# Kernel optimization log

Measured on AMD Instinct MI355X. Metric: run time of the kernel, lower is better.

The kernel has to match this reference:

```python
import jax, jax.numpy as jnp
import numpy as np
import math

C = 256
NUM_CLASSES = 80
NUM_CONVS = 4
GROUPS = 32
LEVEL_SHAPES = [(100, 152), (50, 76), (25, 38), (13, 19), (7, 10)]
BATCH = 2


def conv2d(x, w, b):
    # x: [N,C,H,W], w: [O,I,3,3] -> SAME padding, stride 1
    y = jax.lax.conv_general_dilated(x, w, window_strides=(1, 1), padding='SAME',
                                     dimension_numbers=('NCHW', 'OIHW', 'NCHW'))
    return y + b[None, :, None, None]


def group_norm(x, w, b, groups=GROUPS, eps=1e-5):
    N, Ch, H, W = x.shape
    xg = x.reshape(N, groups, Ch // groups, H, W)
    mu = jnp.mean(xg, axis=(2, 3, 4), keepdims=True)
    var = jnp.var(xg, axis=(2, 3, 4), keepdims=True)
    xg = (xg - mu) * jax.lax.rsqrt(var + eps)
    x = xg.reshape(N, Ch, H, W)
    return x * w[None, :, None, None] + b[None, :, None, None]


def tower(x, cw, cb, gw, gb):
    for i in range(NUM_CONVS):
        x = jax.nn.relu(group_norm(conv2d(x, cw[i], cb[i]), gw[i], gb[i]))
    return x


def flatten_head(y, c):
    # [N, A*c, H, W] -> [N, H*W*A, c]  (matches view/permute/reshape in torch)
    N, AC, H, W = y.shape
    A = AC // c
    return y.reshape(N, A, c, H, W).transpose(0, 3, 4, 1, 2).reshape(N, H * W * A, c)


def setup_inputs() -> dict:
    key = jax.random.key(0)
    ks = iter(jax.random.split(key, 64))
    inp = {}
    for i, (h, w) in enumerate(LEVEL_SHAPES):
        inp[f"feat{i}"] = jax.random.normal(next(ks), (BATCH, C, h, w), jnp.float32)
    def cw(shape):  # conv weights init std=0.01 as in torch module
        return jax.random.normal(next(ks), shape, jnp.float32) * 0.01
    inp["cls_conv_w"] = cw((NUM_CONVS, C, C, 3, 3))
    inp["cls_conv_b"] = jnp.zeros((NUM_CONVS, C), jnp.float32)
    inp["cls_gn_w"] = jnp.ones((NUM_CONVS, C), jnp.float32)
    inp["cls_gn_b"] = jnp.zeros((NUM_CONVS, C), jnp.float32)
    inp["cls_out_w"] = cw((NUM_CLASSES, C, 3, 3))
    inp["cls_out_b"] = jnp.full((NUM_CLASSES,), -math.log(99.0), jnp.float32)  # prior prob 0.01
    inp["reg_conv_w"] = cw((NUM_CONVS, C, C, 3, 3))
    inp["reg_conv_b"] = jnp.zeros((NUM_CONVS, C), jnp.float32)
    inp["reg_gn_w"] = jnp.ones((NUM_CONVS, C), jnp.float32)
    inp["reg_gn_b"] = jnp.zeros((NUM_CONVS, C), jnp.float32)
    for name, oc in [("bbox", 4), ("ctr", 1), ("dim", 3), ("ori", 1), ("kp", 16), ("depth", 1)]:
        inp[f"{name}_w"] = cw((oc, C, 3, 3))
        inp[f"{name}_b"] = jnp.zeros((oc,), jnp.float32)
    return inp


def reference(feat0, feat1, feat2, feat3, feat4,
              cls_conv_w, cls_conv_b, cls_gn_w, cls_gn_b, cls_out_w, cls_out_b,
              reg_conv_w, reg_conv_b, reg_gn_w, reg_gn_b,
              bbox_w, bbox_b, ctr_w, ctr_b, dim_w, dim_b,
              ori_w, ori_b, kp_w, kp_b, depth_w, depth_b):
    feats = [feat0, feat1, feat2, feat3, feat4]
    cls_all, bbox_all, ctr_all, dim_all, ori_all, kp_all, depth_all = ([] for _ in range(7))
    for f in feats:
        cf = tower(f, cls_conv_w, cls_conv_b, cls_gn_w, cls_gn_b)
        cls_all.append(flatten_head(conv2d(cf, cls_out_w, cls_out_b), NUM_CLASSES))
        rf = tower(f, reg_conv_w, reg_conv_b, reg_gn_w, reg_gn_b)
        bbox_all.append(flatten_head(jax.nn.relu(conv2d(rf, bbox_w, bbox_b)), 4))
        ctr_all.append(flatten_head(conv2d(rf, ctr_w, ctr_b), 1))
        dim_all.append(flatten_head(conv2d(rf, dim_w, dim_b), 3))
        ori_all.append(flatten_head(conv2d(rf, ori_w, ori_b), 1))
        kp_all.append(flatten_head(conv2d(rf, kp_w, kp_b), 16))
        depth_all.append(flatten_head(conv2d(rf, depth_w, depth_b), 1))
    cat = lambda xs: jnp.concatenate(xs, axis=1)
    return (cat(cls_all), cat(bbox_all), cat(ctr_all), cat(dim_all),
            cat(ori_all), cat(kp_all), cat(depth_all))
```

## Files before the change

### kernel.cpp

```cpp
#include <hip/hip_runtime.h>
#include <stdint.h>

typedef unsigned short ushort_t;
typedef __bf16 bf16x8 __attribute__((ext_vector_type(8)));
typedef float f32x4 __attribute__((ext_vector_type(4)));

#define TOTAL_HW 20267
#define PTOT 21267

__constant__ int d_RB[26] = {3242720,3242720,3242720,3242720, 3404856, 3445390,3445390,3445390,
                             3566992, 3607526,3607526,3607526,3607526,3607526,3607526,3607526,3607526,
                             3607526,3607526,3607526,3607526,3607526,3607526,3607526,3607526, 4256070};
__constant__ int d_RM[26] = {4,4,4,4, 1, 3,3,3, 1, 16,16,16,16,16,16,16,16,16,16,16,16,16,16,16,16, 1};
__constant__ int d_RC[26] = {0,1,2,3, 0, 0,1,2, 0, 0,1,2,3,4,5,6,7,8,9,10,11,12,13,14,15, 0};

__constant__ int F_TC[6]   = {0,238,298,314,318,320};
__constant__ int F_TL[5]   = {119,30,8,2,1};
__constant__ int F_W[5]    = {152,76,38,19,10};
__constant__ int F_HW[5]   = {15200,3800,950,247,70};
__constant__ int F_PB[5]   = {0,15708,19764,20844,21159};
__constant__ int F_LOFF[5] = {0,15200,19000,19950,20197};
__constant__ int F_PC[6]   = {0,508,764,894,962,1000};
__constant__ int F_H[5]    = {100,50,25,13,7};

__device__ __forceinline__ ushort_t f2bf(float f) {
    union { float f; uint32_t i; } x; x.f = f;
    uint32_t r = x.i + 0x7fffu + ((x.i >> 16) & 1u);
    return (ushort_t)(r >> 16);
}
__device__ __forceinline__ float bf2f(ushort_t u) {
    union { uint32_t i; float f; } x; x.i = ((uint32_t)u) << 16; return x.f;
}
__device__ __forceinline__ void gld16(const ushort_t* g, ushort_t* lds) {
    __builtin_amdgcn_global_load_lds((const __attribute__((address_space(1))) void*)g,
                                     (__attribute__((address_space(3))) void*)lds, 16, 0, 0);
}

__global__ __launch_bounds__(256) void wprep_k(
    const float* __restrict__ cw, const float* __restrict__ rw,
    const float* __restrict__ cls_out_w,
    const float* bbox_w, const float* ctr_w, const float* dim_w,
    const float* ori_w,  const float* kp_w,  const float* depth_w,
    const float* bbox_b, const float* ctr_b, const float* dim_b,
    const float* ori_b,  const float* kp_b,  const float* depth_b,
    ushort_t* __restrict__ TowerWtAll, ushort_t* __restrict__ WtCls,
    ushort_t* __restrict__ WtReg, float* __restrict__ RegBias,
    float* __restrict__ Stats)
{
    int bid = blockIdx.x;
    if (bid < 2048) {
        int id = bid * 256 + threadIdx.x;
        int g = id >> 16;
        int oc = (id >> 8) & 255, ic = id & 255;
        const float* base = (g >= 4) ? rw : cw;
        int L = g & 3;
        const float* s = base + (size_t)L * 589824 + (size_t)(oc * 256 + ic) * 9;
        ushort_t* d = TowerWtAll + (size_t)g * 589824 + oc * 256 + ic;
        #pragma unroll
        for (int t = 0; t < 9; t++) d[t * 65536] = f2bf(s[t]);
    } else if (bid < 2176) {
        int id = (bid - 2048) * 256 + threadIdx.x;
        int oc = id >> 8, ic = id & 255;
        ushort_t* d = WtCls + oc * 256 + ic;
        if (oc < 80) {
            const float* s = cls_out_w + (size_t)(oc * 256 + ic) * 9;
            #pragma unroll
            for (int t = 0; t < 9; t++) d[t * 32768] = f2bf(s[t]);
        } else {
            #pragma unroll
            for (int t = 0; t < 9; t++) d[t * 32768] = 0;
        }
    } else {
        int id = (bid - 2176) * 256 + threadIdx.x;
        if (id < 5120) Stats[id] = 0.f;
        int oc = id >> 8, ic = id & 255;
        ushort_t* d = WtReg + oc * 256 + ic;
        if (oc < 26) {
            const float* s; int c;
            if (oc < 4)       { s = bbox_w;  c = oc; }
            else if (oc < 5)  { s = ctr_w;   c = 0; }
            else if (oc < 8)  { s = dim_w;   c = oc - 5; }
            else if (oc < 9)  { s = ori_w;   c = 0; }
            else if (oc < 25) { s = kp_w;    c = oc - 9; }
            else              { s = depth_w; c = 0; }
            const float* sp = s + (size_t)(c * 256 + ic) * 9;
            #pragma unroll
            for (int t = 0; t < 9; t++) d[t * 32768] = f2bf(sp[t]);
        } else {
            #pragma unroll
            for (int t = 0; t < 9; t++) d[t * 32768] = 0;
        }
        if (id < 26) {
            const float* b; int c;
            if (id < 4)       { b = bbox_b;  c = id; }
            else if (id < 5)  { b = ctr_b;   c = 0; }
            else if (id < 8)  { b = dim_b;   c = id - 5; }
            else if (id < 9)  { b = ori_b;   c = 0; }
            else if (id < 25) { b = kp_b;    c = id - 9; }
            else              { b = depth_b; c = 0; }
            RegBias[id] = b[c];
        }
    }
}

__global__ __launch_bounds__(256) void packF_k(
    const float* f0, const float* f1, const float* f2,
    const float* f3, const float* f4, ushort_t* __restrict__ S,
    ushort_t* __restrict__ pb1, ushort_t* __restrict__ pb2, ushort_t* __restrict__ pb3)
{
    int bid = blockIdx.x;
    if (bid >= 2552) {
        int u = (bid - 2552) * 256 + threadIdx.x;
        if (u >= 256000) return;
        int chunk = u & 31; u >>= 5;
        int buf = u & 3; u >>= 2;
        int n = (u >= 1000) ? 1 : 0; int pidx = u - n * 1000;
        int l = 0;
        #pragma unroll
        for (int i = 1; i < 5; i++) if (pidx >= F_PC[i]) l = i;
        int q = pidx - F_PC[l];
        int W = F_W[l], H = F_H[l], Wp = W + 2;
        int py, px;
        if (q < Wp) { py = 0; px = q; }
        else if (q < 2 * Wp) { py = H + 1; px = q - Wp; }
        else { int q2 = q - 2 * Wp; py = 1 + (q2 >> 1); px = (q2 & 1) ? (Wp - 1) : 0; }
        ushort_t* base = S;
        if (buf == 1) base = pb1; else if (buf == 2) base = pb2; else if (buf == 3) base = pb3;
        *(uint4*)(base + ((size_t)n * PTOT + F_PB[l] + py * Wp + px) * 256 + chunk * 8) = uint4{0u,0u,0u,0u};
        return;
    }
    __shared__ ushort_t tile[64][65];
    const int PCUM[6] = {0, 1904, 2384, 2504, 2536, 2552};
    const int PT[5]   = {238, 60, 15, 4, 2};
    int l = 0;
    #pragma unroll
    for (int i = 1; i < 5; i++) if (bid >= PCUM[i]) l = i;
    int r = bid - PCUM[l];
    int per_n = PT[l] * 4;
    int n = (r >= per_n) ? 1 : 0; r -= n * per_n;
    int pb = r >> 2, cb = r & 3;
    const float* fs = f0;
    if (l == 1) fs = f1; else if (l == 2) fs = f2; else if (l == 3) fs = f3; else if (l == 4) fs = f4;
    int HW = F_HW[l], W = F_W[l], Wp = W + 2;
    int p0 = pb * 64, c0 = cb * 64;
    int t = threadIdx.x;
    bool full = (p0 + 64 <= HW);
    if (full && l <= 1) {
        #pragma unroll
        for (int i = 0; i < 4; i++) {
            int idx = i * 256 + t; int cl = idx >> 4, pw = idx & 15;
            const float* rp = fs + (size_t)(n * 256 + c0 + cl) * HW + p0 + pw * 4;
            float4 v = *(const float4*)rp;
            tile[cl][pw * 4 + 0] = f2bf(v.x);
            tile[cl][pw * 4 + 1] = f2bf(v.y);
            tile[cl][pw * 4 + 2] = f2bf(v.z);
            tile[cl][pw * 4 + 3] = f2bf(v.w);
        }
    } else if (full && (l == 2 || l == 4)) {
        #pragma unroll
        for (int i = 0; i < 8; i++) {
            int idx = i * 256 + t; int cl = idx >> 5, pw = idx & 31;
            const float* rp = fs + (size_t)(n * 256 + c0 + cl) * HW + p0 + pw * 2;
            float2 v = *(const float2*)rp;
            tile[cl][pw * 2 + 0] = f2bf(v.x);
            tile[cl][pw * 2 + 1] = f2bf(v.y);
        }
    } else {
        #pragma unroll
        for (int i = 0; i < 16; i++) {
            int idx = i * 256 + t; int cl = idx >> 6, pl = idx & 63;
            int p = p0 + pl; ushort_t v = 0;
            if (p < HW) v = f2bf(fs[(size_t)(n * 256 + c0 + cl) * HW + p]);
            tile[cl][pl] = v;
        }
    }
    __syncthreads();
    ushort_t* ob = S + ((size_t)n * PTOT + F_PB[l]) * 256;
    #pragma unroll
    for (int i = 0; i < 16; i++) {
        int idx = i * 256 + t; int pl = idx >> 6, cl = idx & 63;
        int p = p0 + pl;
        if (p < HW) {
            int y = p / W, x = p - y * W;
            ob[((y + 1) * Wp + (x + 1)) * 256 + c0 + cl] = tile[cl][pl];
        }
    }
}

__global__ __launch_bounds__(512, 4) void convT_k(
    const ushort_t* __restrict__ srcC, const ushort_t* __restrict__ srcR,
    ushort_t* __restrict__ dstC, ushort_t* __restrict__ dstR,
    const ushort_t* __restrict__ wtAll,
    const float* __restrict__ biasC, const float* __restrict__ biasR,
    float* __restrict__ stats, int L)
{
    __shared__ __align__(16) ushort_t SH[32768];

    int gid = blockIdx.x;
    int xcd = gid & 7, idx = gid >> 3;
    int bid = xcd * 40 + (idx >> 2);
    int oc0 = (idx & 1) * 128;
    int tw = (idx >> 1) & 1;

    const ushort_t* src = tw ? srcR : srcC;
    ushort_t* dst = tw ? dstR : dstC;
    const ushort_t* wt = wtAll + (size_t)(tw * 4 + L) * 589824;
    const float* bias = (tw ? biasR : biasC) + L * 256;

    int l = 0;
    #pragma unroll
    for (int i = 1; i < 5; i++) if (bid >= F_TC[i]) l = i;
    int r = bid - F_TC[l];
    int tl = F_TL[l];
    int n = (r >= tl) ? 1 : 0; int tile = r - n * tl;
    int W = F_W[l], HW = F_HW[l], Wp = W + 2;
    int px0 = tile * 128;
    const ushort_t* sbase = src + ((size_t)n * PTOT + F_PB[l]) * 256;
    ushort_t* obase = dst + ((size_t)n * PTOT + F_PB[l]) * 256;

    int tid = threadIdx.x, wv = tid >> 6, ln = tid & 63;
    int wr = (wv >> 1) & 1, wc = wv & 1, kh = wv >> 2;

    int aoff, boff;
    {
        int rloc = wv * 16 + (ln >> 2);
        int p = px0 + rloc; if (p > HW - 1) p = HW - 1;
        int y = p / W, x = p - y * W;
        int c = ((ln & 3) - (rloc >> 1)) & 3;
        aoff = ((y + 1) * Wp + (x + 1)) * 256 + c * 8;
        boff = (oc0 + rloc) * 256 + c * 8;
    }

    auto stage = [&](int it, int b) {
        int tp = it >> 2, q = it & 3;
        int ky = tp / 3, kx = tp - ky * 3;
        int tapo = ((ky - 1) * Wp + (kx - 1)) * 256 + (q << 6);
        const ushort_t* wtap = wt + tp * 65536 + (q << 6);
        gld16(sbase + aoff + tapo,      &SH[b * 8192 + wv * 512]);
        gld16(sbase + aoff + tapo + 32, &SH[b * 8192 + 4096 + wv * 512]);
        gld16(wtap + boff,      &SH[16384 + b * 8192 + wv * 512]);
        gld16(wtap + boff + 32, &SH[16384 + b * 8192 + 4096 + wv * 512]);
    };

    f32x4 acc[4][4];
    #pragma unroll
    for (int mi = 0; mi < 4; mi++)
        #pragma unroll
        for (int ni = 0; ni < 4; ni++) acc[mi][ni] = f32x4{0.f, 0.f, 0.f, 0.f};

    stage(0, 0);

    #pragma unroll 2
    for (int it = 0; it < 36; ++it) {
        asm volatile("s_waitcnt vmcnt(0) lgkmcnt(0)\n\ts_barrier" ::: "memory");
        if (it + 1 < 36) stage(it + 1, (it + 1) & 1);
        int b = it & 1;
        bf16x8 af[4], bg[4];
        #pragma unroll
        for (int mi = 0; mi < 4; mi++) {
            int rA = wr * 64 + mi * 16 + (ln & 15);
            int ch = ((ln >> 4) + (rA >> 1)) & 3;
            af[mi] = *(const bf16x8*)&SH[b * 8192 + kh * 4096 + rA * 32 + ch * 8];
        }
        #pragma unroll
        for (int ni = 0; ni < 4; ni++) {
            int rB = wc * 64 + ni * 16 + (ln & 15);
            int ch = ((ln >> 4) + (rB >> 1)) & 3;
            bg[ni] = *(const bf16x8*)&SH[16384 + b * 8192 + kh * 4096 + rB * 32 + ch * 8];
        }
        __builtin_amdgcn_s_setprio(1);
        #pragma unroll
        for (int mi = 0; mi < 4; mi++)
            #pragma unroll
            for (int ni = 0; ni < 4; ni++)
                acc[mi][ni] = __builtin_amdgcn_mfma_f32_16x16x32_bf16(af[mi], bg[ni], acc[mi][ni], 0, 0, 0);
        __builtin_amdgcn_s_setprio(0);
    }

    __syncthreads();
    f32x4* F4 = (f32x4*)SH;
    int prt = wv ^ 4;
    if (kh == 0) {
        #pragma unroll
        for (int mi = 0; mi < 4; mi++) {
            F4[wv * 512 + ln * 8 + ((mi * 2 + 0) ^ (ln & 7))] = acc[mi][2];
            F4[wv * 512 + ln * 8 + ((mi * 2 + 1) ^ (ln & 7))] = acc[mi][3];
        }
    } else {
        #pragma unroll
        for (int mi = 0; mi < 4; mi++) {
            F4[wv * 512 + ln * 8 + ((mi * 2 + 0) ^ (ln & 7))] = acc[mi][0];
            F4[wv * 512 + ln * 8 + ((mi * 2 + 1) ^ (ln & 7))] = acc[mi][1];
        }
    }
    __syncthreads();
    f32x4 eacc[4][2];
    if (kh == 0) {
        #pragma unroll
        for (int mi = 0; mi < 4; mi++) {
            eacc[mi][0] = acc[mi][0] + F4[prt * 512 + ln * 8 + ((mi * 2 + 0) ^ (ln & 7))];
            eacc[mi][1] = acc[mi][1] + F4[prt * 512 + ln * 8 + ((mi * 2 + 1) ^ (ln & 7))];
        }
    } else {
        #pragma unroll
        for (int mi = 0; mi < 4; mi++) {
            eacc[mi][0] = acc[mi][2] + F4[prt * 512 + ln * 8 + ((mi * 2 + 0) ^ (ln & 7))];
            eacc[mi][1] = acc[mi][3] + F4[prt * 512 + ln * 8 + ((mi * 2 + 1) ^ (ln & 7))];
        }
    }

    #pragma unroll
    for (int h = 0; h < 2; h++) {
        int oc = oc0 + wc * 64 + (kh * 2 + h) * 16 + (ln & 15);
        float bv = bias[oc];
        float s = 0.f, q = 0.f;
        #pragma unroll
        for (int mi = 0; mi < 4; mi++) {
            int pb = px0 + wr * 64 + mi * 16 + ((ln >> 4) << 2);
            if (pb < HW) {
                int y = pb / W, x = pb - y * W;
                #pragma unroll
                for (int rr2 = 0; rr2 < 4; rr2++) {
                    int p = pb + rr2;
                    if (p < HW) {
                        float v = eacc[mi][h][rr2] + bv;
                        obase[((y + 1) * Wp + (x + 1)) * 256 + oc] = f2bf(v);
                        s += v; q += v * v;
                    }
                    x++; if (x == W) { x = 0; y++; }
                }
            }
        }
        s += __shfl_xor(s, 16, 64); q += __shfl_xor(q, 16, 64);
        s += __shfl_xor(s, 32, 64); q += __shfl_xor(q, 32, 64);
        s += __shfl_xor(s, 1, 64);  q += __shfl_xor(q, 1, 64);
        s += __shfl_xor(s, 2, 64);  q += __shfl_xor(q, 2, 64);
        s += __shfl_xor(s, 4, 64);  q += __shfl_xor(q, 4, 64);
        if (ln == 0 || ln == 8) {
            int g = (oc0 + wc * 64 + (kh * 2 + h) * 16 + (ln & 8)) >> 3;
            float* st = stats + (size_t)((tw * 4 + L) * 5 + l) * 128 + (n * 32 + g) * 2;
            atomicAdd(st, s); atomicAdd(st + 1, q);
        }
    }
}

__global__ __launch_bounds__(512, 4) void convH_k(
    const ushort_t* __restrict__ srcC, const ushort_t* __restrict__ srcR,
    const ushort_t* __restrict__ wtC, const ushort_t* __restrict__ wtR,
    const float* __restrict__ biasC, const float* __restrict__ biasR,
    float* __restrict__ outF)
{
    __shared__ __align__(16) ushort_t SH[32768];

    int gid = blockIdx.x;
    int xcd = gid & 7, idx = gid >> 3;
    int bid = xcd * 40 + (idx >> 1);
    int mode = idx & 1;

    const ushort_t* src = mode ? srcR : srcC;
    const ushort_t* wt  = mode ? wtR  : wtC;
    const float* bias   = mode ? biasR : biasC;

    int l = 0;
    #pragma unroll
    for (int i = 1; i < 5; i++) if (bid >= F_TC[i]) l = i;
    int r = bid - F_TC[l];
    int tl = F_TL[l];
    int n = (r >= tl) ? 1 : 0; int tile = r - n * tl;
    int W = F_W[l], HW = F_HW[l], Wp = W + 2;
    int px0 = tile * 128;
    const ushort_t* sbase = src + ((size_t)n * PTOT + F_PB[l]) * 256;

    int tid = threadIdx.x, wv = tid >> 6, ln = tid & 63;
    int wr = (wv >> 1) & 1, wc = wv & 1, kh = wv >> 2;
    bool active = (mode == 0) || (wc == 0);
    bool stageB = (mode == 0) || (wv < 2);

    int aoff, boff;
    {
        int rloc = wv * 16 + (ln >> 2);
        int p = px0 + rloc; if (p > HW - 1) p = HW - 1;
        int y = p / W, x = p - y * W;
        int c = ((ln & 3) - (rloc >> 1)) & 3;
        aoff = ((y + 1) * Wp + (x + 1)) * 256 + c * 8;
        boff = rloc * 256 + c * 8;
    }

    auto stage = [&](int it, int b) {
        int tp = it >> 2, q = it & 3;
        int ky = tp / 3, kx = tp - ky * 3;
        int tapo = ((ky - 1) * Wp + (kx - 1)) * 256 + (q << 6);
        const ushort_t* wtap = wt + tp * 32768 + (q << 6);
        gld16(sbase + aoff + tapo,      &SH[b * 8192 + wv * 512]);
        gld16(sbase + aoff + tapo + 32, &SH[b * 8192 + 4096 + wv * 512]);
        if (stageB) {
            gld16(wtap + boff,      &SH[16384 + b * 8192 + wv * 512]);
            gld16(wtap + boff + 32, &SH[16384 + b * 8192 + 4096 + wv * 512]);
        }
    };

    f32x4 acc[4][4];
    #pragma unroll
    for (int mi = 0; mi < 4; mi++)
        #pragma unroll
        for (int ni = 0; ni < 4; ni++) acc[mi][ni] = f32x4{0.f, 0.f, 0.f, 0.f};

    stage(0, 0);

    #pragma unroll 2
    for (int it = 0; it < 36; ++it) {
        asm volatile("s_waitcnt vmcnt(0) lgkmcnt(0)\n\ts_barrier" ::: "memory");
        if (it + 1 < 36) stage(it + 1, (it + 1) & 1);
        int b = it & 1;
        if (active) {
            bf16x8 af[4], bg[4];
            #pragma unroll
            for (int mi = 0; mi < 4; mi++) {
                int rA = wr * 64 + mi * 16 + (ln & 15);
                int ch = ((ln >> 4) + (rA >> 1)) & 3;
                af[mi] = *(const bf16x8*)&SH[b * 8192 + kh * 4096 + rA * 32 + ch * 8];
            }
            #pragma unroll
            for (int ni = 0; ni < 4; ni++) {
                int rB = wc * 64 + ni * 16 + (ln & 15);
                int ch = ((ln >> 4) + (rB >> 1)) & 3;
                bg[ni] = *(const bf16x8*)&SH[16384 + b * 8192 + kh * 4096 + rB * 32 + ch * 8];
            }
            __builtin_amdgcn_s_setprio(1);
            #pragma unroll
            for (int mi = 0; mi < 4; mi++)
                #pragma unroll
                for (int ni = 0; ni < 4; ni++)
                    acc[mi][ni] = __builtin_amdgcn_mfma_f32_16x16x32_bf16(af[mi], bg[ni], acc[mi][ni], 0, 0, 0);
            __builtin_amdgcn_s_setprio(0);
        }
    }

    __syncthreads();
    f32x4* F4 = (f32x4*)SH;
    int prt = wv ^ 4;
    if (active) {
        if (kh == 0) {
            #pragma unroll
            for (int mi = 0; mi < 4; mi++) {
                F4[wv * 512 + ln * 8 + ((mi * 2 + 0) ^ (ln & 7))] = acc[mi][2];
                F4[wv * 512 + ln * 8 + ((mi * 2 + 1) ^ (ln & 7))] = acc[mi][3];
            }
        } else {
            #pragma unroll
            for (int mi = 0; mi < 4; mi++) {
                F4[wv * 512 + ln * 8 + ((mi * 2 + 0) ^ (ln & 7))] = acc[mi][0];
                F4[wv * 512 + ln * 8 + ((mi * 2 + 1) ^ (ln & 7))] = acc[mi][1];
            }
        }
    }
    __syncthreads();
    f32x4 eacc[4][2];
    if (kh == 0) {
        #pragma unroll
        for (int mi = 0; mi < 4; mi++) {
            eacc[mi][0] = acc[mi][0] + F4[prt * 512 + ln * 8 + ((mi * 2 + 0) ^ (ln & 7))];
            eacc[mi][1] = acc[mi][1] + F4[prt * 512 + ln * 8 + ((mi * 2 + 1) ^ (ln & 7))];
        }
    } else {
        #pragma unroll
        for (int mi = 0; mi < 4; mi++) {
            eacc[mi][0] = acc[mi][2] + F4[prt * 512 + ln * 8 + ((mi * 2 + 0) ^ (ln & 7))];
            eacc[mi][1] = acc[mi][3] + F4[prt * 512 + ln * 8 + ((mi * 2 + 1) ^ (ln & 7))];
        }
    }

    #pragma unroll
    for (int h = 0; h < 2; h++) {
        int oc = wc * 64 + (kh * 2 + h) * 16 + (ln & 15);
        bool valid = mode ? (oc < 26) : (oc < 80);
        if (valid) {
            float bv = bias[oc];
            int rb = 0, rm = 80, rc = oc; bool rl = false;
            if (mode) { rb = d_RB[oc]; rm = d_RM[oc]; rc = d_RC[oc]; rl = (oc < 4); }
            #pragma unroll
            for (int mi = 0; mi < 4; mi++) {
                int pb = px0 + wr * 64 + mi * 16 + ((ln >> 4) << 2);
                #pragma unroll
                for (int rr2 = 0; rr2 < 4; rr2++) {
                    int p = pb + rr2;
                    if (p < HW) {
                        float v = eacc[mi][h][rr2] + bv;
                        if (rl) v = fmaxf(v, 0.f);
                        int pg = n * TOTAL_HW + F_LOFF[l] + p;
                        outF[rb + (size_t)pg * rm + rc] = v;
                    }
                }
            }
        }
    }
}

__global__ __launch_bounds__(256) void normF_k(
    ushort_t* __restrict__ bufC, ushort_t* __restrict__ bufR,
    const float* __restrict__ stats,
    const float* __restrict__ gwC, const float* __restrict__ gwR,
    const float* __restrict__ gbC, const float* __restrict__ gbR, int L)
{
    int u = blockIdx.x * 256 + threadIdx.x;
    if (u >= 2594176) return;
    int tw = (u >= 1297088) ? 1 : 0; u -= tw * 1297088;
    int n = (u >= 648544) ? 1 : 0; u -= n * 648544;
    int cp = u >> 5, g = u & 31;
    int l = 0;
    #pragma unroll
    for (int i = 1; i < 5; i++) if (cp >= F_LOFF[i]) l = i;
    int p = cp - F_LOFF[l];
    int W = F_W[l], HW = F_HW[l];
    int y = p / W, x = p - y * W;
    const float* st = stats + (size_t)((tw * 4 + L) * 5 + l) * 128 + (n * 32 + g) * 2;
    float cnt = 8.0f * (float)HW;
    float mean = st[0] / cnt;
    float var = st[1] / cnt - mean * mean;
    float inv = rsqrtf(fmaxf(var, 0.f) + 1e-5f);
    const float* gw = (tw ? gwR : gwC) + L * 256 + g * 8;
    const float* gb = (tw ? gbR : gbC) + L * 256 + g * 8;
    ushort_t* buf = tw ? bufR : bufC;
    ushort_t* ptr = buf + (((size_t)n * PTOT + F_PB[l]) + (y + 1) * (W + 2) + (x + 1)) * 256 + g * 8;
    uint4 din = *(const uint4*)ptr;
    uint4 dout;
    const ushort_t* xi = (const ushort_t*)&din;
    ushort_t* oi = (ushort_t*)&dout;
    #pragma unroll
    for (int i = 0; i < 8; i++) {
        float v = (bf2f(xi[i]) - mean) * inv * gw[i] + gb[i];
        oi[i] = f2bf(fmaxf(v, 0.f));
    }
    *(uint4*)ptr = dout;
}


extern "C" void kernel_launch(void* const* d_in, const int* in_sizes, int n_in,
                              void* d_out, int out_size, void* d_ws, size_t ws_size,
                              hipStream_t stream) {
    const float* feats[5] = {(const float*)d_in[0], (const float*)d_in[1],
                             (const float*)d_in[2], (const float*)d_in[3],
                             (const float*)d_in[4]};
    const float* cls_conv_w = (const float*)d_in[5];
    const float* cls_conv_b = (const float*)d_in[6];
    const float* cls_gn_w   = (const float*)d_in[7];
    const float* cls_gn_b   = (const float*)d_in[8];
    const float* cls_out_w  = (const float*)d_in[9];
    const float* cls_out_b  = (const float*)d_in[10];
    const float* reg_conv_w = (const float*)d_in[11];
    const float* reg_conv_b = (const float*)d_in[12];
    const float* reg_gn_w   = (const float*)d_in[13];
    const float* reg_gn_b   = (const float*)d_in[14];

    char* wsb = (char*)d_ws;
    float* Stats     = (float*)wsb;
    float* RegBias   = (float*)(wsb + 20480);
    ushort_t* TowerWtAll = (ushort_t*)(wsb + 20608);
    ushort_t* WtCls  = (ushort_t*)(wsb + 9457792);
    ushort_t* WtReg  = (ushort_t*)(wsb + 10047616);
    ushort_t* S  = (ushort_t*)(wsb + 10637440);
    ushort_t* Ac = (ushort_t*)(wsb + 32414848);
    ushort_t* Ar = (ushort_t*)(wsb + 54192256);
    ushort_t* Br = (ushort_t*)(wsb + 75969664);
    float* outf  = (float*)d_out;

    wprep_k<<<2304, 256, 0, stream>>>(
        cls_conv_w, reg_conv_w, cls_out_w,
        (const float*)d_in[15], (const float*)d_in[17], (const float*)d_in[19],
        (const float*)d_in[21], (const float*)d_in[23], (const float*)d_in[25],
        (const float*)d_in[16], (const float*)d_in[18], (const float*)d_in[20],
        (const float*)d_in[22], (const float*)d_in[24], (const float*)d_in[26],
        TowerWtAll, WtCls, WtReg, RegBias, Stats);

    packF_k<<<3552, 256, 0, stream>>>(feats[0], feats[1], feats[2], feats[3], feats[4],
                                      S, Ac, Ar, Br);

    ushort_t* sc[4] = {S,  Ac, S,  Ac};
    ushort_t* dc[4] = {Ac, S,  Ac, S };
    ushort_t* sr[4] = {S,  Ar, Br, Ar};
    ushort_t* dr[4] = {Ar, Br, Ar, Br};
    for (int L = 0; L < 4; L++) {
        convT_k<<<1280, 512, 0, stream>>>(
            sc[L], sr[L], dc[L], dr[L], TowerWtAll, cls_conv_b, reg_conv_b, Stats, L);
        normF_k<<<10134, 256, 0, stream>>>(
            dc[L], dr[L], Stats, cls_gn_w, reg_gn_w, cls_gn_b, reg_gn_b, L);
    }
    convH_k<<<640, 512, 0, stream>>>(S, Br, WtCls, WtReg, cls_out_b, RegBias, outf);
}
```

Baseline: 775.1 us.

## Load conv weight fragments directly from global memory in MFMA-ready layout

Weights are repacked at prep time into a fragment-ordered layout (tap, k-chunk, half, 8-element sub-chunk, oc, element), so each lane can load its bf16x8 B fragment straight from global memory. The B operand is no longer staged through LDS in either the tower or head conv kernels. This removes LDS writes and reads for weights and frees shared memory bandwidth. In exchange, each iteration issues global loads that sit directly on the MFMA critical path, with only L1/L2 caching to hide their latency.

```diff
diff --git a/kernel.cpp b/kernel.cpp
--- a/kernel.cpp
+++ b/kernel.cpp
@@ -55,13 +55,15 @@
         const float* base = (g >= 4) ? rw : cw;
         int L = g & 3;
         const float* s = base + (size_t)L * 589824 + (size_t)(oc * 256 + ic) * 9;
-        ushort_t* d = TowerWtAll + (size_t)g * 589824 + oc * 256 + ic;
+        int q = ic >> 6, kh = (ic >> 5) & 1, s8 = (ic >> 3) & 3, e = ic & 7;
+        ushort_t* d = TowerWtAll + (size_t)g * 589824 + (((q * 2 + kh) * 4 + s8) * 2048) + oc * 8 + e;
         #pragma unroll
         for (int t = 0; t < 9; t++) d[t * 65536] = f2bf(s[t]);
     } else if (bid < 2176) {
         int id = (bid - 2048) * 256 + threadIdx.x;
         int oc = id >> 8, ic = id & 255;
-        ushort_t* d = WtCls + oc * 256 + ic;
+        int q = ic >> 6, kh = (ic >> 5) & 1, s8 = (ic >> 3) & 3, e = ic & 7;
+        ushort_t* d = WtCls + (((q * 2 + kh) * 4 + s8) * 1024) + oc * 8 + e;
         if (oc < 80) {
             const float* s = cls_out_w + (size_t)(oc * 256 + ic) * 9;
             #pragma unroll
@@ -74,7 +76,8 @@
         int id = (bid - 2176) * 256 + threadIdx.x;
         if (id < 5120) Stats[id] = 0.f;
         int oc = id >> 8, ic = id & 255;
-        ushort_t* d = WtReg + oc * 256 + ic;
+        int q = ic >> 6, kh = (ic >> 5) & 1, s8 = (ic >> 3) & 3, e = ic & 7;
+        ushort_t* d = WtReg + (((q * 2 + kh) * 4 + s8) * 1024) + oc * 8 + e;
         if (oc < 26) {
             const float* s; int c;
             if (oc < 4)       { s = bbox_w;  c = oc; }
@@ -221,25 +224,22 @@
     int tid = threadIdx.x, wv = tid >> 6, ln = tid & 63;
     int wr = (wv >> 1) & 1, wc = wv & 1, kh = wv >> 2;
 
-    int aoff, boff;
+    int aoff;
     {
         int rloc = wv * 16 + (ln >> 2);
         int p = px0 + rloc; if (p > HW - 1) p = HW - 1;
         int y = p / W, x = p - y * W;
         int c = ((ln & 3) - (rloc >> 1)) & 3;
         aoff = ((y + 1) * Wp + (x + 1)) * 256 + c * 8;
-        boff = (oc0 + rloc) * 256 + c * 8;
-    }
-
-    auto stage = [&](int it, int b) {
+    }
+    int fragoff = (ln >> 4) * 2048;
+
+    auto stageA = [&](int it, int b) {
         int tp = it >> 2, q = it & 3;
         int ky = tp / 3, kx = tp - ky * 3;
         int tapo = ((ky - 1) * Wp + (kx - 1)) * 256 + (q << 6);
-        const ushort_t* wtap = wt + tp * 65536 + (q << 6);
         gld16(sbase + aoff + tapo,      &SH[b * 8192 + wv * 512]);
         gld16(sbase + aoff + tapo + 32, &SH[b * 8192 + 4096 + wv * 512]);
-        gld16(wtap + boff,      &SH[16384 + b * 8192 + wv * 512]);
-        gld16(wtap + boff + 32, &SH[16384 + b * 8192 + 4096 + wv * 512]);
     };
 
     f32x4 acc[4][4];
@@ -248,25 +248,25 @@
         #pragma unroll
         for (int ni = 0; ni < 4; ni++) acc[mi][ni] = f32x4{0.f, 0.f, 0.f, 0.f};
 
-    stage(0, 0);
+    stageA(0, 0);
 
     #pragma unroll 2
     for (int it = 0; it < 36; ++it) {
         asm volatile("s_waitcnt vmcnt(0) lgkmcnt(0)\n\ts_barrier" ::: "memory");
-        if (it + 1 < 36) stage(it + 1, (it + 1) & 1);
+        int tp = it >> 2, q = it & 3;
+        const ushort_t* wB = wt + (size_t)(((tp * 4 + q) * 2 + kh) * 4) * 2048 + fragoff;
+        bf16x8 bg[4];
+        #pragma unroll
+        for (int ni = 0; ni < 4; ni++)
+            bg[ni] = *(const bf16x8*)&wB[(oc0 + wc * 64 + ni * 16 + (ln & 15)) * 8];
+        if (it + 1 < 36) stageA(it + 1, (it + 1) & 1);
         int b = it & 1;
-        bf16x8 af[4], bg[4];
+        bf16x8 af[4];
         #pragma unroll
         for (int mi = 0; mi < 4; mi++) {
             int rA = wr * 64 + mi * 16 + (ln & 15);
             int ch = ((ln >> 4) + (rA >> 1)) & 3;
             af[mi] = *(const bf16x8*)&SH[b * 8192 + kh * 4096 + rA * 32 + ch * 8];
-        }
-        #pragma unroll
-        for (int ni = 0; ni < 4; ni++) {
-            int rB = wc * 64 + ni * 16 + (ln & 15);
-            int ch = ((ln >> 4) + (rB >> 1)) & 3;
-            bg[ni] = *(const bf16x8*)&SH[16384 + b * 8192 + kh * 4096 + rB * 32 + ch * 8];
         }
         __builtin_amdgcn_s_setprio(1);
         #pragma unroll
@@ -374,29 +374,23 @@
     int tid = threadIdx.x, wv = tid >> 6, ln = tid & 63;
     int wr = (wv >> 1) & 1, wc = wv & 1, kh = wv >> 2;
     bool active = (mode == 0) || (wc == 0);
-    bool stageB = (mode == 0) || (wv < 2);
-
-    int aoff, boff;
+
+    int aoff;
     {
         int rloc = wv * 16 + (ln >> 2);
         int p = px0 + rloc; if (p > HW - 1) p = HW - 1;
         int y = p / W, x = p - y * W;
         int c = ((ln & 3) - (rloc >> 1)) & 3;
         aoff = ((y + 1) * Wp + (x + 1)) * 256 + c * 8;
-        boff = rloc * 256 + c * 8;
-    }
-
-    auto stage = [&](int it, int b) {
+    }
+    int fragoff = (ln >> 4) * 1024;
+
+    auto stageA = [&](int it, int b) {
         int tp = it >> 2, q = it & 3;
         int ky = tp / 3, kx = tp - ky * 3;
         int tapo = ((ky - 1) * Wp + (kx - 1)) * 256 + (q << 6);
-        const ushort_t* wtap = wt + tp * 32768 + (q << 6);
         gld16(sbase + aoff + tapo,      &SH[b * 8192 + wv * 512]);
         gld16(sbase + aoff + tapo + 32, &SH[b * 8192 + 4096 + wv * 512]);
-        if (stageB) {
-            gld16(wtap + boff,      &SH[16384 + b * 8192 + wv * 512]);
-            gld16(wtap + boff + 32, &SH[16384 + b * 8192 + 4096 + wv * 512]);
-        }
     };
 
     f32x4 acc[4][4];
@@ -405,26 +399,26 @@
         #pragma unroll
         for (int ni = 0; ni < 4; ni++) acc[mi][ni] = f32x4{0.f, 0.f, 0.f, 0.f};
 
-    stage(0, 0);
+    stageA(0, 0);
 
     #pragma unroll 2
     for (int it = 0; it < 36; ++it) {
         asm volatile("s_waitcnt vmcnt(0) lgkmcnt(0)\n\ts_barrier" ::: "memory");
-        if (it + 1 < 36) stage(it + 1, (it + 1) & 1);
+        int tp = it >> 2, q = it & 3;
+        if (it + 1 < 36) stageA(it + 1, (it + 1) & 1);
         int b = it & 1;
         if (active) {
-            bf16x8 af[4], bg[4];
+            const ushort_t* wB = wt + (size_t)(((tp * 4 + q) * 2 + kh) * 4) * 1024 + fragoff;
+            bf16x8 bg[4];
+            #pragma unroll
+            for (int ni = 0; ni < 4; ni++)
+                bg[ni] = *(const bf16x8*)&wB[(wc * 64 + ni * 16 + (ln & 15)) * 8];
+            bf16x8 af[4];
             #pragma unroll
             for (int mi = 0; mi < 4; mi++) {
                 int rA = wr * 64 + mi * 16 + (ln & 15);
                 int ch = ((ln >> 4) + (rA >> 1)) & 3;
                 af[mi] = *(const bf16x8*)&SH[b * 8192 + kh * 4096 + rA * 32 + ch * 8];
-            }
-            #pragma unroll
-            for (int ni = 0; ni < 4; ni++) {
-                int rB = wc * 64 + ni * 16 + (ln & 15);
-                int ch = ((ln >> 4) + (rB >> 1)) & 3;
-                bg[ni] = *(const bf16x8*)&SH[16384 + b * 8192 + kh * 4096 + rB * 32 + ch * 8];
             }
             __builtin_amdgcn_s_setprio(1);
             #pragma unroll
```

New measurement: 858.3 us. +10.7%, slower.
